# Performance work log

Hardware: AMD Instinct MI355X
Metric: run time of the kernel (lower is better)

## Reference

```python
import jax, jax.numpy as jnp
import numpy as np

C = 256
NH = 8
DH = C // NH
LN_EPS = 1e-5
COS_EPS = 1e-6


def _ln(x, w, b):
    m = x.mean(axis=-1, keepdims=True)
    v = ((x - m) ** 2).mean(axis=-1, keepdims=True)
    return (x - m) / jnp.sqrt(v + LN_EPS) * w + b


def _mha(q_in, kv_in, in_proj_w, in_proj_b, out_proj_w, out_proj_b):
    # q_in, kv_in: [P, S, C]. torch.nn.MultiheadAttention (batch_first).
    P, S, _ = q_in.shape
    q = q_in @ in_proj_w[:C].T + in_proj_b[:C]
    k = kv_in @ in_proj_w[C:2 * C].T + in_proj_b[C:2 * C]
    v = kv_in @ in_proj_w[2 * C:].T + in_proj_b[2 * C:]
    q = q.reshape(P, S, NH, DH)
    k = k.reshape(P, S, NH, DH)
    v = v.reshape(P, S, NH, DH)
    scores = jnp.einsum('pqhd,pkhd->phqk', q, k) / jnp.sqrt(jnp.asarray(DH, q.dtype))
    attn = jax.nn.softmax(scores, axis=-1)
    ctx = jnp.einsum('phqk,pkhd->pqhd', attn, v).reshape(P, S, C)
    return ctx @ out_proj_w.T + out_proj_b


def setup_inputs() -> dict:
    key = jax.random.key(0)
    ks = jax.random.split(key, 8)
    s = 0.02
    return {
        'z_sem': jax.random.normal(ks[0], (16, C, 32, 32), jnp.float32),
        'pair_indices': jnp.arange(16, dtype=jnp.int32).reshape(8, 2),
        'ln_w': jnp.ones((C,), jnp.float32),
        'ln_b': jnp.zeros((C,), jnp.float32),
        'in_proj_w': jax.random.normal(ks[1], (3 * C, C), jnp.float32) * s,
        'in_proj_b': jnp.zeros((3 * C,), jnp.float32),
        'out_proj_w': jax.random.normal(ks[2], (C, C), jnp.float32) * s,
        'out_proj_b': jnp.zeros((C,), jnp.float32),
        'res_scale': jnp.asarray(0.1, jnp.float32),
        'gate_scale': jnp.asarray(2.0, jnp.float32),
        'mlp_ln_w': jnp.ones((C,), jnp.float32),
        'mlp_ln_b': jnp.zeros((C,), jnp.float32),
        'mlp_w1': jax.random.normal(ks[3], (4 * C, C), jnp.float32) * s,
        'mlp_b1': jnp.zeros((4 * C,), jnp.float32),
        'mlp_w2': jax.random.normal(ks[4], (C, 4 * C), jnp.float32) * s,
        'mlp_b2': jnp.zeros((C,), jnp.float32),
    }


def reference(z_sem, pair_indices, ln_w, ln_b, in_proj_w, in_proj_b,
              out_proj_w, out_proj_b, res_scale, gate_scale,
              mlp_ln_w, mlp_ln_b, mlp_w1, mlp_b1, mlp_w2, mlp_b2):
    B, Cc, Hh, Ww = z_sem.shape
    S = Hh * Ww
    tokens = z_sem.reshape(B, Cc, S).transpose(0, 2, 1)  # [B, S, C]

    i_idx = pair_indices[:, 0]
    j_idx = pair_indices[:, 1]
    base_i = tokens[i_idx]  # [P, S, C]
    base_j = tokens[j_idx]

    q_i = _ln(base_i, ln_w, ln_b)
    q_j = _ln(base_j, ln_w, ln_b)

    cross_i = _mha(q_i, q_j, in_proj_w, in_proj_b, out_proj_w, out_proj_b)
    cross_j = _mha(q_j, q_i, in_proj_w, in_proj_b, out_proj_w, out_proj_b)

    # cosine similarity between mean-pooled normed tokens
    mi = q_i.mean(axis=1)  # [P, C]
    mj = q_j.mean(axis=1)
    ni = mi / jnp.maximum(jnp.linalg.norm(mi, axis=-1, keepdims=True), COS_EPS)
    nj = mj / jnp.maximum(jnp.linalg.norm(mj, axis=-1, keepdims=True), COS_EPS)
    sim = (ni * nj).sum(axis=-1)  # [P]
    gate = jax.nn.sigmoid(gate_scale * sim)  # [P]

    g = (res_scale * gate)[:, None, None]
    new_i = base_i + g * cross_i
    new_j = base_j + g * cross_j

    def _mlp(x):
        h = _ln(x, mlp_ln_w, mlp_ln_b)
        h = jax.nn.gelu(h @ mlp_w1.T + mlp_b1, approximate=False)
        return h @ mlp_w2.T + mlp_b2

    new_i = new_i + _mlp(new_i)
    new_j = new_j + _mlp(new_j)

    updated = tokens.at[i_idx].set(new_i).at[j_idx].set(new_j)
    shared = updated.transpose(0, 2, 1).reshape(B, Cc, Hh, Ww)
    return shared, gate, sim
```

## Files before the change

kernel.cpp:

```cpp
#include <hip/hip_runtime.h>
#include <hip/hip_bf16.h>

#define C_ 256
#define S_ 1024
#define NH_ 8
#define DH_ 32
#define NSIDE 16
#define MTOT (NSIDE * S_)

typedef __hip_bfloat16 bf16;
typedef short bf8_t __attribute__((ext_vector_type(8)));
typedef float f4_t __attribute__((ext_vector_type(4)));

#if __has_builtin(__builtin_amdgcn_exp2f)
#define QSCALE 0.25504167f
__device__ __forceinline__ float fastexp(float x) { return __builtin_amdgcn_exp2f(x); }
#else
#define QSCALE 0.17677669529663689f
__device__ __forceinline__ float fastexp(float x) { return __expf(x); }
#endif

__device__ __forceinline__ float b2f(bf16 x) { return __bfloat162float(x); }
__device__ __forceinline__ bf16 f2b(float x) { return __float2bfloat16(x); }
__device__ __forceinline__ unsigned short f2bu(float x) {
    bf16 h = f2b(x);
    return *reinterpret_cast<unsigned short*>(&h);
}
__device__ __forceinline__ unsigned pack_trunc(float a, float b) {
    return __builtin_amdgcn_perm(__float_as_uint(b), __float_as_uint(a), 0x07060302u);
}

__device__ __forceinline__ float block_sum(float v, float* red) {
#pragma unroll
    for (int off = 1; off < 64; off <<= 1) v += __shfl_xor(v, off);
    __syncthreads();
    if ((threadIdx.x & 63) == 0) red[threadIdx.x >> 6] = v;
    __syncthreads();
    return red[0] + red[1] + red[2] + red[3];
}

__device__ __forceinline__ void packone(const float* __restrict__ src, bf16* __restrict__ dst,
                                        int i, int kshift) {
    int n = i >> kshift, k = i & ((1 << kshift) - 1);
    size_t a = ((size_t)((n >> 4) * (1 << (kshift - 5)) + (k >> 5)) << 9) +
               (((k >> 3) & 3) << 7) + ((n & 15) << 3) + (k & 7);
    dst[a] = f2b(src[i]);
}

__global__ void pack4(const float* __restrict__ a, bf16* __restrict__ oa,
                      const float* __restrict__ b, bf16* __restrict__ ob,
                      const float* __restrict__ c, bf16* __restrict__ oc,
                      const float* __restrict__ d, bf16* __restrict__ od) {
    int i = blockIdx.x * blockDim.x + threadIdx.x;
    if (i < 196608) { packone(a, oa, i, 8); return; }
    i -= 196608;
    if (i < 65536) { packone(b, ob, i, 8); return; }
    i -= 65536;
    if (i < 262144) { packone(c, oc, i, 8); return; }
    i -= 262144;
    if (i < 262144) packone(d, od, i, 10);
}

__global__ __launch_bounds__(256) void ln_tokens_g(const float* __restrict__ src,
                                                   const int* __restrict__ pair,
                                                   const float* __restrict__ w,
                                                   const float* __restrict__ b,
                                                   bf16* __restrict__ dst) {
    __shared__ float psum[4][64], psq[4][64], mean_s[64], rstd_s[64];
    __shared__ float wb[512];
    int sb = blockIdx.x, u = blockIdx.y;
    int bi = pair[u];
    int tid = threadIdx.x;
    wb[tid] = w[tid];
    wb[256 + tid] = b[tid];
    int sl = tid & 63, cp = tid >> 6;
    int s = sb * 64 + sl;
    const float* zb = src + (size_t)bi * C_ * S_ + s;
    float sum = 0.f, sq = 0.f;
    for (int c = cp * 64; c < cp * 64 + 64; ++c) {
        float x = zb[(size_t)c * S_];
        sum += x;
        sq += x * x;
    }
    psum[cp][sl] = sum;
    psq[cp][sl] = sq;
    __syncthreads();
    if (tid < 64) {
        float sm = psum[0][tid] + psum[1][tid] + psum[2][tid] + psum[3][tid];
        float q2 = psq[0][tid] + psq[1][tid] + psq[2][tid] + psq[3][tid];
        float mean = sm * (1.0f / C_);
        float var = q2 * (1.0f / C_) - mean * mean;
        mean_s[tid] = mean;
        rstd_s[tid] = rsqrtf(var + 1e-5f);
    }
    __syncthreads();
    float mean = mean_s[sl], rstd = rstd_s[sl];
    int m = u * S_ + s;
    size_t tile8 = (size_t)(m >> 4) * 8;
    for (int c8 = 0; c8 < 64; c8 += 8) {
        int c = cp * 64 + c8;
        bf8_t pk;
#pragma unroll
        for (int j = 0; j < 8; ++j) {
            float x = zb[(size_t)(c + j) * S_];
            float y = (x - mean) * rstd * wb[c + j] + wb[256 + c + j];
            pk[j] = (short)f2bu(y);
        }
        *reinterpret_cast<bf8_t*>(dst + ((tile8 + (c >> 5)) << 9) +
                                  (((c >> 3) & 3) << 7) + ((m & 15) << 3)) = pk;
    }
}

__global__ __launch_bounds__(256) void mean_partial(const bf16* __restrict__ qln,
                                                    float* __restrict__ partial) {
    int u = blockIdx.y, sy = blockIdx.x;
    int c = threadIdx.x;
    float sum = 0.f;
    int s0 = sy * 128;
    int inner = (((c >> 3) & 3) << 7) + (c & 7);
    for (int a = 0; a < 8; ++a) {
        const bf16* p = qln + ((((size_t)u * 64 + (s0 >> 4) + a) * 8 + (c >> 5)) << 9) + inner;
#pragma unroll
        for (int bq = 0; bq < 16; ++bq) sum += b2f(p[bq << 3]);
    }
    partial[(u * 8 + sy) * C_ + c] = sum;
}

__global__ __launch_bounds__(256) void gate_kernel(const float* __restrict__ partial,
                                                   const float* __restrict__ gate_scale,
                                                   float* __restrict__ gatef,
                                                   float* __restrict__ out_gate,
                                                   float* __restrict__ out_sim) {
    __shared__ float red[4];
    int p = blockIdx.x, c = threadIdx.x;
    float mi = 0.f, mj = 0.f;
    for (int sy = 0; sy < 8; ++sy) {
        mi += partial[((2 * p) * 8 + sy) * C_ + c];
        mj += partial[((2 * p + 1) * 8 + sy) * C_ + c];
    }
    mi *= (1.f / S_);
    mj *= (1.f / S_);
    float ii = block_sum(mi * mi, red);
    float jj = block_sum(mj * mj, red);
    float ij = block_sum(mi * mj, red);
    if (c == 0) {
        float ni = fmaxf(sqrtf(ii), 1e-6f);
        float nj = fmaxf(sqrtf(jj), 1e-6f);
        float sim = ij / (ni * nj);
        float gate = 1.f / (1.f + expf(-gate_scale[0] * sim));
        gatef[p] = gate;
        out_gate[p] = gate;
        out_sim[p] = sim;
    }
}

__global__ __launch_bounds__(256) void gemm_qkv(
    const bf16* __restrict__ Apk, const bf16* __restrict__ Wpk, const float* __restrict__ bias,
    bf16* __restrict__ qpk, bf16* __restrict__ kpk, bf16* __restrict__ vpk) {
    int tid = threadIdx.x;
    int wv = tid >> 6, lane = tid & 63;
    int ln15 = lane & 15, quad = lane >> 4;
    int idx = blockIdx.x * 4 + wv;
    int mt = idx / 12, nt = idx % 12;
    int m0 = mt * 64, n0 = nt * 64;

    f4_t acc[4][4];
#pragma unroll
    for (int i = 0; i < 4; ++i)
#pragma unroll
        for (int j = 0; j < 4; ++j) acc[i][j] = (f4_t)(0.0f);

    const bf16* Ab = Apk + ((size_t)mt << 14) + lane * 8;
    const bf16* Wb = Wpk + ((size_t)nt << 14) + lane * 8;

    bf8_t a0[4], w0[4], a1[4], w1[4];
#pragma unroll
    for (int i = 0; i < 4; ++i) {
        a0[i] = *reinterpret_cast<const bf8_t*>(Ab + ((size_t)(i * 8) << 9));
        w0[i] = *reinterpret_cast<const bf8_t*>(Wb + ((size_t)(i * 8) << 9));
    }
    for (int kch = 0; kch < 8; kch += 2) {
#pragma unroll
        for (int i = 0; i < 4; ++i) {
            a1[i] = *reinterpret_cast<const bf8_t*>(Ab + ((size_t)(i * 8 + kch + 1) << 9));
            w1[i] = *reinterpret_cast<const bf8_t*>(Wb + ((size_t)(i * 8 + kch + 1) << 9));
        }
#pragma unroll
        for (int i = 0; i < 4; ++i)
#pragma unroll
            for (int j = 0; j < 4; ++j)
                acc[i][j] = __builtin_amdgcn_mfma_f32_16x16x32_bf16(a0[i], w0[j], acc[i][j], 0, 0, 0);
        if (kch + 2 < 8) {
#pragma unroll
            for (int i = 0; i < 4; ++i) {
                a0[i] = *reinterpret_cast<const bf8_t*>(Ab + ((size_t)(i * 8 + kch + 2) << 9));
                w0[i] = *reinterpret_cast<const bf8_t*>(Wb + ((size_t)(i * 8 + kch + 2) << 9));
            }
        }
#pragma unroll
        for (int i = 0; i < 4; ++i)
#pragma unroll
            for (int j = 0; j < 4; ++j)
                acc[i][j] = __builtin_amdgcn_mfma_f32_16x16x32_bf16(a1[i], w1[j], acc[i][j], 0, 0, 0);
    }

#pragma unroll
    for (int i = 0; i < 4; ++i) {
#pragma unroll
        for (int j = 0; j < 4; ++j) {
            int coln = n0 + j * 16 + ln15;
            float bs = bias[coln];
            int row0 = m0 + i * 16 + quad * 4;
            int u = row0 >> 10, s0v = row0 & 1023;
            if (coln < 256) {
                int h = coln >> 5, d = coln & 31;
                bf16* qp = qpk + (((size_t)u * 8 + h) * 1024 + s0v) * 32 + d;
#pragma unroll
                for (int r = 0; r < 4; ++r)
                    qp[r * 32] = f2b((acc[i][j][r] + bs) * QSCALE);
            } else if (coln < 512) {
                int c = coln - 256, h = c >> 5, d = c & 31;
                bf16* kp = kpk + (((size_t)u * 8 + h) * 1024 + s0v) * 32 + d;
#pragma unroll
                for (int r = 0; r < 4; ++r)
                    kp[r * 32] = f2b(acc[i][j][r] + bs);
            } else {
                int c = coln - 512, h = c >> 5, d = c & 31;
                ushort4 pk;
#pragma unroll
                for (int r = 0; r < 4; ++r)
                    ((unsigned short*)&pk)[r] = f2bu(acc[i][j][r] + bs);
                *reinterpret_cast<ushort4*>(
                    vpk + ((((size_t)u * 8 + h) * 32 + (s0v >> 5)) * 32 + d) * 32 + (s0v & 31)) = pk;
            }
        }
    }
}

__global__ __launch_bounds__(256) void attn_mfma(const bf16* __restrict__ qpk,
                                                 const bf16* __restrict__ kpk,
                                                 const bf16* __restrict__ vpk,
                                                 bf16* __restrict__ ctx) {
    __shared__ __align__(16) short smem[4 * 2304];
    int tid = threadIdx.x;
    int wv = tid >> 6, lane = tid & 63;
    int ln15 = lane & 15, quad = lane >> 4;
    int bid = blockIdx.x;
    int g = bid >> 6, rem = bid & 63;
    int qb = rem >> 3, xcd = rem & 7;
    int uh = g * 8 + xcd;
    int u = uh >> 3, h = uh & 7, up = u ^ 3 ^ 2;
    up = (u ^ 1);
    int q0 = qb * 128 + wv * 32;
    short* PL = smem + wv * 2304;

    const bf16* Qb = qpk + (size_t)uh * 32768;
    const bf16* Kb = kpk + ((size_t)(up * 8 + h)) * 32768;
    const bf16* Vb = vpk + ((size_t)(up * 8 + h)) * 32768;

    bf8_t qf[2];
#pragma unroll
    for (int qt = 0; qt < 2; ++qt)
        qf[qt] = *reinterpret_cast<const bf8_t*>(Qb + (size_t)(q0 + qt * 16 + ln15) * 32 + quad * 8);

    bf8_t ones;
#pragma unroll
    for (int t = 0; t < 8; ++t) ones[t] = (short)0x3F80;

    const bf16* kp = Kb + ln15 * 32 + quad * 8;
    const bf16* vp = Vb + ln15 * 32 + quad * 8;
    short* plw = PL + ln15 * 72 + quad * 4;
    const short* plr = PL + ln15 * 72 + quad * 8;

    f4_t o[2][2];
#pragma unroll
    for (int i = 0; i < 2; ++i)
#pragma unroll
        for (int j = 0; j < 2; ++j) o[i][j] = (f4_t)(0.0f);
    f4_t lacc[2];
    lacc[0] = (f4_t)(0.0f);
    lacc[1] = (f4_t)(0.0f);
    f4_t zf = (f4_t)(0.0f);

    for (int it = 0; it < 16; ++it) {
        int k0 = it * 64;
        bf8_t kf[4], vt[2][2];
#pragma unroll
        for (int t = 0; t < 4; ++t)
            kf[t] = *reinterpret_cast<const bf8_t*>(kp + (size_t)(k0 + t * 16) * 32);
#pragma unroll
        for (int kc = 0; kc < 2; ++kc)
#pragma unroll
            for (int dh = 0; dh < 2; ++dh)
                vt[kc][dh] = *reinterpret_cast<const bf8_t*>(vp + (size_t)(it * 2 + kc) * 1024 + dh * 512);

        f4_t st[4][2];
#pragma unroll
        for (int kh = 0; kh < 4; ++kh)
#pragma unroll
            for (int qt = 0; qt < 2; ++qt)
                st[kh][qt] = __builtin_amdgcn_mfma_f32_16x16x32_bf16(kf[kh], qf[qt], zf, 0, 0, 0);

#pragma unroll
        for (int qt = 0; qt < 2; ++qt) {
#pragma unroll
            for (int kh = 0; kh < 4; ++kh) {
                float e0 = fastexp(st[kh][qt][0]);
                float e1 = fastexp(st[kh][qt][1]);
                float e2 = fastexp(st[kh][qt][2]);
                float e3 = fastexp(st[kh][qt][3]);
                uint2 pk;
                pk.x = pack_trunc(e0, e1);
                pk.y = pack_trunc(e2, e3);
                *reinterpret_cast<uint2*>(plw + qt * 1152 + kh * 16) = pk;
            }
        }
#pragma unroll
        for (int qt = 0; qt < 2; ++qt) {
#pragma unroll
            for (int kc = 0; kc < 2; ++kc) {
                bf8_t pf = *reinterpret_cast<const bf8_t*>(plr + qt * 1152 + kc * 32);
                o[0][qt] = __builtin_amdgcn_mfma_f32_16x16x32_bf16(vt[kc][0], pf, o[0][qt], 0, 0, 0);
                o[1][qt] = __builtin_amdgcn_mfma_f32_16x16x32_bf16(vt[kc][1], pf, o[1][qt], 0, 0, 0);
                lacc[qt] = __builtin_amdgcn_mfma_f32_16x16x32_bf16(ones, pf, lacc[qt], 0, 0, 0);
            }
        }
    }

#pragma unroll
    for (int qt = 0; qt < 2; ++qt) {
        float inv = 1.f / lacc[qt][0];
        size_t base = ((size_t)(u * S_ + q0 + qt * 16 + ln15)) * C_ + h * DH_;
#pragma unroll
        for (int dh = 0; dh < 2; ++dh) {
            ushort4 pk;
            pk.x = f2bu(o[dh][qt][0] * inv);
            pk.y = f2bu(o[dh][qt][1] * inv);
            pk.z = f2bu(o[dh][qt][2] * inv);
            pk.w = f2bu(o[dh][qt][3] * inv);
            *reinterpret_cast<ushort4*>(ctx + base + dh * 16 + quad * 4) = pk;
        }
    }
}

__global__ __launch_bounds__(512) void fused_tail(
    const bf16* __restrict__ ctx, const bf16* __restrict__ wout,
    const float* __restrict__ bout, const float* __restrict__ z,
    const int* __restrict__ pair, const float* __restrict__ gatef,
    const float* __restrict__ res_scale,
    const float* __restrict__ lnw, const float* __restrict__ lnb,
    const bf16* __restrict__ w1b, const float* __restrict__ b1,
    const bf16* __restrict__ w2b, const float* __restrict__ b2,
    float* __restrict__ outp) {
    __shared__ __align__(16) short Xs[32][264];
    __shared__ __align__(16) short CHs[32][264];
    __shared__ float ssum[8][32], ssq[8][32], smean[32], srstd[32];

    int tid = threadIdx.x;
    int wv = tid >> 6, lane = tid & 63;
    int ln15 = lane & 15, quad = lane >> 4;
    int u = blockIdx.x >> 5;
    int s0 = (blockIdx.x & 31) * 32;
    int bi = pair[u];
    float g = res_scale[0] * gatef[u >> 1];
    int c0 = wv * 32;

    {
        int row = tid >> 4, col = (tid & 15) * 16;
        const bf16* src = ctx + ((size_t)(u * S_ + s0 + row)) * 256 + col;
        *reinterpret_cast<bf8_t*>(&CHs[row][col]) = *reinterpret_cast<const bf8_t*>(src);
        *reinterpret_cast<bf8_t*>(&CHs[row][col + 8]) = *reinterpret_cast<const bf8_t*>(src + 8);
    }
    __syncthreads();

    f4_t yacc[2][2];
#pragma unroll
    for (int i = 0; i < 2; ++i)
#pragma unroll
        for (int j = 0; j < 2; ++j) yacc[i][j] = (f4_t)(0.0f);
    {
        const bf16* Wb = wout + (((size_t)(wv * 2) * 8) << 9) + lane * 8;
#pragma unroll
        for (int kch = 0; kch < 8; ++kch) {
            bf8_t wf[2], xf[2];
#pragma unroll
            for (int i = 0; i < 2; ++i)
                wf[i] = *reinterpret_cast<const bf8_t*>(Wb + ((size_t)(i * 8 + kch) << 9));
#pragma unroll
            for (int j = 0; j < 2; ++j)
                xf[j] = *reinterpret_cast<const bf8_t*>(&CHs[j * 16 + ln15][kch * 32 + quad * 8]);
#pragma unroll
            for (int i = 0; i < 2; ++i)
#pragma unroll
                for (int j = 0; j < 2; ++j)
                    yacc[i][j] = __builtin_amdgcn_mfma_f32_16x16x32_bf16(wf[i], xf[j], yacc[i][j], 0, 0, 0);
        }
    }
    float psum[2] = {0.f, 0.f}, psq[2] = {0.f, 0.f};
#pragma unroll
    for (int i = 0; i < 2; ++i) {
#pragma unroll
        for (int r = 0; r < 4; ++r) {
            int c = c0 + i * 16 + quad * 4 + r;
            float bs = bout[c];
            const float* zr = z + ((size_t)bi * C_ + c) * S_ + s0;
#pragma unroll
            for (int j = 0; j < 2; ++j) {
                int sl = j * 16 + ln15;
                float y = zr[sl] + g * (yacc[i][j][r] + bs);
                yacc[i][j][r] = y;
                psum[j] += y;
                psq[j] += y * y;
            }
        }
    }
#pragma unroll
    for (int j = 0; j < 2; ++j) {
        psum[j] += __shfl_xor(psum[j], 16);
        psum[j] += __shfl_xor(psum[j], 32);
        psq[j] += __shfl_xor(psq[j], 16);
        psq[j] += __shfl_xor(psq[j], 32);
    }
    if (quad == 0) {
#pragma unroll
        for (int j = 0; j < 2; ++j) {
            ssum[wv][j * 16 + ln15] = psum[j];
            ssq[wv][j * 16 + ln15] = psq[j];
        }
    }
    __syncthreads();
    if (tid < 32) {
        float sm = 0.f, q2 = 0.f;
#pragma unroll
        for (int w = 0; w < 8; ++w) {
            sm += ssum[w][tid];
            q2 += ssq[w][tid];
        }
        float mean = sm * (1.0f / C_);
        float var = q2 * (1.0f / C_) - mean * mean;
        smean[tid] = mean;
        srstd[tid] = rsqrtf(var + 1e-5f);
    }
    __syncthreads();
#pragma unroll
    for (int j = 0; j < 2; ++j) {
        int sl = j * 16 + ln15;
        float mean = smean[sl], rstd = srstd[sl];
#pragma unroll
        for (int i = 0; i < 2; ++i) {
            ushort4 pk;
#pragma unroll
            for (int r = 0; r < 4; ++r) {
                int c = c0 + i * 16 + quad * 4 + r;
                float xv = (yacc[i][j][r] - mean) * rstd * lnw[c] + lnb[c];
                ((unsigned short*)&pk)[r] = f2bu(xv);
            }
            *reinterpret_cast<ushort4*>(&Xs[sl][c0 + i * 16 + quad * 4]) = pk;
        }
    }
    __syncthreads();

    f4_t acc2[2][2];
#pragma unroll
    for (int i = 0; i < 2; ++i)
#pragma unroll
        for (int j = 0; j < 2; ++j) acc2[i][j] = (f4_t)(0.0f);

    for (int pass = 0; pass < 4; ++pass) {
        f4_t hacc[2][2];
#pragma unroll
        for (int i = 0; i < 2; ++i)
#pragma unroll
            for (int j = 0; j < 2; ++j) hacc[i][j] = (f4_t)(0.0f);
        {
            const bf16* W1p = w1b + (((size_t)(pass * 16 + wv * 2) * 8) << 9) + lane * 8;
#pragma unroll
            for (int kch = 0; kch < 8; ++kch) {
                bf8_t wf[2], xf[2];
#pragma unroll
                for (int i = 0; i < 2; ++i)
                    wf[i] = *reinterpret_cast<const bf8_t*>(W1p + ((size_t)(i * 8 + kch) << 9));
#pragma unroll
                for (int j = 0; j < 2; ++j)
                    xf[j] = *reinterpret_cast<const bf8_t*>(&Xs[j * 16 + ln15][kch * 32 + quad * 8]);
#pragma unroll
                for (int i = 0; i < 2; ++i)
#pragma unroll
                    for (int j = 0; j < 2; ++j)
                        hacc[i][j] = __builtin_amdgcn_mfma_f32_16x16x32_bf16(wf[i], xf[j], hacc[i][j], 0, 0, 0);
            }
        }
#pragma unroll
        for (int j = 0; j < 2; ++j) {
#pragma unroll
            for (int i = 0; i < 2; ++i) {
                ushort4 pk;
#pragma unroll
                for (int r = 0; r < 4; ++r) {
                    int hg = pass * 256 + c0 + i * 16 + quad * 4 + r;
                    float v = hacc[i][j][r] + b1[hg];
                    float ge = 0.5f * v * (1.f + erff(v * 0.70710678118f));
                    ((unsigned short*)&pk)[r] = f2bu(ge);
                }
                *reinterpret_cast<ushort4*>(&CHs[j * 16 + ln15][c0 + i * 16 + quad * 4]) = pk;
            }
        }
        __syncthreads();
        {
            const bf16* W2p = w2b + (((size_t)(wv * 2) * 32 + pass * 8) << 9) + lane * 8;
#pragma unroll
            for (int kch = 0; kch < 8; ++kch) {
                bf8_t wf[2], hf[2];
#pragma unroll
                for (int i = 0; i < 2; ++i)
                    wf[i] = *reinterpret_cast<const bf8_t*>(W2p + ((size_t)(i * 32 + kch) << 9));
#pragma unroll
                for (int j = 0; j < 2; ++j)
                    hf[j] = *reinterpret_cast<const bf8_t*>(&CHs[j * 16 + ln15][kch * 32 + quad * 8]);
#pragma unroll
                for (int i = 0; i < 2; ++i)
#pragma unroll
                    for (int j = 0; j < 2; ++j)
                        acc2[i][j] = __builtin_amdgcn_mfma_f32_16x16x32_bf16(wf[i], hf[j], acc2[i][j], 0, 0, 0);
            }
        }
        __syncthreads();
    }

#pragma unroll
    for (int i = 0; i < 2; ++i) {
#pragma unroll
        for (int r = 0; r < 4; ++r) {
            int c = c0 + i * 16 + quad * 4 + r;
            float bs = b2[c];
            float* orow = outp + ((size_t)bi * C_ + c) * S_ + s0;
#pragma unroll
            for (int j = 0; j < 2; ++j)
                orow[j * 16 + ln15] = yacc[i][j][r] + acc2[i][j][r] + bs;
        }
    }
}

extern "C" void kernel_launch(void* const* d_in, const int* in_sizes, int n_in,
                              void* d_out, int out_size, void* d_ws, size_t ws_size,
                              hipStream_t stream) {
    const float* z = (const float*)d_in[0];
    const int* pair = (const int*)d_in[1];
    const float* ln_w = (const float*)d_in[2];
    const float* ln_b = (const float*)d_in[3];
    const float* in_proj_w = (const float*)d_in[4];
    const float* in_proj_b = (const float*)d_in[5];
    const float* out_proj_w = (const float*)d_in[6];
    const float* out_proj_b = (const float*)d_in[7];
    const float* res_scale = (const float*)d_in[8];
    const float* gate_scale = (const float*)d_in[9];
    const float* mlp_ln_w = (const float*)d_in[10];
    const float* mlp_ln_b = (const float*)d_in[11];
    const float* mlp_w1 = (const float*)d_in[12];
    const float* mlp_b1 = (const float*)d_in[13];
    const float* mlp_w2 = (const float*)d_in[14];
    const float* mlp_b2 = (const float*)d_in[15];
    float* out = (float*)d_out;

    char* ws = (char*)d_ws;
    bf16* qln = (bf16*)(ws);
    bf16* qpk = (bf16*)(ws + 8388608);
    bf16* kpk = (bf16*)(ws + 16777216);
    bf16* vpk = (bf16*)(ws + 25165824);
    bf16* ctx = (bf16*)(ws + 33554432);
    bf16* wqkv = (bf16*)(ws + 41943040);
    bf16* wout = (bf16*)(ws + 41943040 + 393216);
    bf16* w1b = (bf16*)(ws + 41943040 + 524288);
    bf16* w2b = (bf16*)(ws + 41943040 + 1048576);
    float* partial = (float*)(ws + 50331648);
    float* gatef = (float*)(ws + 50462720);

    pack4<<<3072, 256, 0, stream>>>(in_proj_w, wqkv, out_proj_w, wout,
                                    mlp_w1, w1b, mlp_w2, w2b);
    ln_tokens_g<<<dim3(16, 16), 256, 0, stream>>>(z, pair, ln_w, ln_b, qln);
    mean_partial<<<dim3(8, 16), 256, 0, stream>>>(qln, partial);
    gate_kernel<<<8, 256, 0, stream>>>(partial, gate_scale, gatef, out + 4194304, out + 4194312);
    gemm_qkv<<<768, 256, 0, stream>>>(qln, wqkv, in_proj_b, qpk, kpk, vpk);
    attn_mfma<<<1024, 256, 0, stream>>>(qpk, kpk, vpk, ctx);
    fused_tail<<<512, 512, 0, stream>>>(ctx, wout, out_proj_b, z, pair, gatef, res_scale,
                                        mlp_ln_w, mlp_ln_b, w1b, mlp_b1, w2b, mlp_b2, out);
}
```

Baseline: 211.1 us.

## Fuse mean pooling into LN kernel and halve attention query tile per block

The LayerNorm kernel now stages its normalized bf16 tile in shared memory and writes per-block channel sums directly, removing the separate mean_partial kernel launch and its re-read of qln. The gate kernel reduces 16 partials instead of 8. The attention kernel processes 16 queries per wave instead of 32 and launches twice as many blocks. This raises parallelism and lowers register and LDS use, but each K/V tile is now loaded twice as often.

```diff
diff --git a/kernel.cpp b/kernel.cpp
--- a/kernel.cpp
+++ b/kernel.cpp
@@ -65,9 +65,11 @@
                                                    const int* __restrict__ pair,
                                                    const float* __restrict__ w,
                                                    const float* __restrict__ b,
-                                                   bf16* __restrict__ dst) {
+                                                   bf16* __restrict__ dst,
+                                                   float* __restrict__ partial) {
     __shared__ float psum[4][64], psq[4][64], mean_s[64], rstd_s[64];
     __shared__ float wb[512];
+    __shared__ __align__(16) short Ys[64][264];
     int sb = blockIdx.x, u = blockIdx.y;
     int bi = pair[u];
     int tid = threadIdx.x;
@@ -106,24 +108,16 @@
             float y = (x - mean) * rstd * wb[c + j] + wb[256 + c + j];
             pk[j] = (short)f2bu(y);
         }
+        *reinterpret_cast<bf8_t*>(&Ys[sl][c]) = pk;
         *reinterpret_cast<bf8_t*>(dst + ((tile8 + (c >> 5)) << 9) +
                                   (((c >> 3) & 3) << 7) + ((m & 15) << 3)) = pk;
     }
-}
-
-__global__ __launch_bounds__(256) void mean_partial(const bf16* __restrict__ qln,
-                                                    float* __restrict__ partial) {
-    int u = blockIdx.y, sy = blockIdx.x;
-    int c = threadIdx.x;
-    float sum = 0.f;
-    int s0 = sy * 128;
-    int inner = (((c >> 3) & 3) << 7) + (c & 7);
-    for (int a = 0; a < 8; ++a) {
-        const bf16* p = qln + ((((size_t)u * 64 + (s0 >> 4) + a) * 8 + (c >> 5)) << 9) + inner;
-#pragma unroll
-        for (int bq = 0; bq < 16; ++bq) sum += b2f(p[bq << 3]);
-    }
-    partial[(u * 8 + sy) * C_ + c] = sum;
+    __syncthreads();
+    float csum = 0.f;
+#pragma unroll 8
+    for (int t = 0; t < 64; ++t)
+        csum += b2f(*reinterpret_cast<const bf16*>(&Ys[t][tid]));
+    partial[((size_t)u * 16 + sb) * C_ + tid] = csum;
 }
 
 __global__ __launch_bounds__(256) void gate_kernel(const float* __restrict__ partial,
@@ -134,9 +128,9 @@
     __shared__ float red[4];
     int p = blockIdx.x, c = threadIdx.x;
     float mi = 0.f, mj = 0.f;
-    for (int sy = 0; sy < 8; ++sy) {
-        mi += partial[((2 * p) * 8 + sy) * C_ + c];
-        mj += partial[((2 * p + 1) * 8 + sy) * C_ + c];
+    for (int sy = 0; sy < 16; ++sy) {
+        mi += partial[((size_t)(2 * p) * 16 + sy) * C_ + c];
+        mj += partial[((size_t)(2 * p + 1) * 16 + sy) * C_ + c];
     }
     mi *= (1.f / S_);
     mj *= (1.f / S_);
@@ -241,27 +235,23 @@
                                                  const bf16* __restrict__ kpk,
                                                  const bf16* __restrict__ vpk,
                                                  bf16* __restrict__ ctx) {
-    __shared__ __align__(16) short smem[4 * 2304];
+    __shared__ __align__(16) short smem[4 * 1152];
     int tid = threadIdx.x;
     int wv = tid >> 6, lane = tid & 63;
     int ln15 = lane & 15, quad = lane >> 4;
     int bid = blockIdx.x;
-    int g = bid >> 6, rem = bid & 63;
+    int g = bid >> 7, rem = bid & 127;
     int qb = rem >> 3, xcd = rem & 7;
     int uh = g * 8 + xcd;
-    int u = uh >> 3, h = uh & 7, up = u ^ 3 ^ 2;
-    up = (u ^ 1);
-    int q0 = qb * 128 + wv * 32;
-    short* PL = smem + wv * 2304;
+    int u = uh >> 3, h = uh & 7, up = u ^ 1;
+    int q0 = qb * 64 + wv * 16;
+    short* PL = smem + wv * 1152;
 
     const bf16* Qb = qpk + (size_t)uh * 32768;
     const bf16* Kb = kpk + ((size_t)(up * 8 + h)) * 32768;
     const bf16* Vb = vpk + ((size_t)(up * 8 + h)) * 32768;
 
-    bf8_t qf[2];
-#pragma unroll
-    for (int qt = 0; qt < 2; ++qt)
-        qf[qt] = *reinterpret_cast<const bf8_t*>(Qb + (size_t)(q0 + qt * 16 + ln15) * 32 + quad * 8);
+    bf8_t qf = *reinterpret_cast<const bf8_t*>(Qb + (size_t)(q0 + ln15) * 32 + quad * 8);
 
     bf8_t ones;
 #pragma unroll
@@ -272,14 +262,10 @@
     short* plw = PL + ln15 * 72 + quad * 4;
     const short* plr = PL + ln15 * 72 + quad * 8;
 
-    f4_t o[2][2];
-#pragma unroll
-    for (int i = 0; i < 2; ++i)
-#pragma unroll
-        for (int j = 0; j < 2; ++j) o[i][j] = (f4_t)(0.0f);
-    f4_t lacc[2];
-    lacc[0] = (f4_t)(0.0f);
-    lacc[1] = (f4_t)(0.0f);
+    f4_t o[2];
+    o[0] = (f4_t)(0.0f);
+    o[1] = (f4_t)(0.0f);
+    f4_t lacc = (f4_t)(0.0f);
     f4_t zf = (f4_t)(0.0f);
 
     for (int it = 0; it < 16; ++it) {
@@ -294,52 +280,41 @@
             for (int dh = 0; dh < 2; ++dh)
                 vt[kc][dh] = *reinterpret_cast<const bf8_t*>(vp + (size_t)(it * 2 + kc) * 1024 + dh * 512);
 
-        f4_t st[4][2];
+        f4_t st[4];
 #pragma unroll
         for (int kh = 0; kh < 4; ++kh)
-#pragma unroll
-            for (int qt = 0; qt < 2; ++qt)
-                st[kh][qt] = __builtin_amdgcn_mfma_f32_16x16x32_bf16(kf[kh], qf[qt], zf, 0, 0, 0);
-
-#pragma unroll
-        for (int qt = 0; qt < 2; ++qt) {
-#pragma unroll
-            for (int kh = 0; kh < 4; ++kh) {
-                float e0 = fastexp(st[kh][qt][0]);
-                float e1 = fastexp(st[kh][qt][1]);
-                float e2 = fastexp(st[kh][qt][2]);
-                float e3 = fastexp(st[kh][qt][3]);
-                uint2 pk;
-                pk.x = pack_trunc(e0, e1);
-                pk.y = pack_trunc(e2, e3);
-                *reinterpret_cast<uint2*>(plw + qt * 1152 + kh * 16) = pk;
-            }
-        }
-#pragma unroll
-        for (int qt = 0; qt < 2; ++qt) {
-#pragma unroll
-            for (int kc = 0; kc < 2; ++kc) {
-                bf8_t pf = *reinterpret_cast<const bf8_t*>(plr + qt * 1152 + kc * 32);
-                o[0][qt] = __builtin_amdgcn_mfma_f32_16x16x32_bf16(vt[kc][0], pf, o[0][qt], 0, 0, 0);
-                o[1][qt] = __builtin_amdgcn_mfma_f32_16x16x32_bf16(vt[kc][1], pf, o[1][qt], 0, 0, 0);
-                lacc[qt] = __builtin_amdgcn_mfma_f32_16x16x32_bf16(ones, pf, lacc[qt], 0, 0, 0);
-            }
-        }
-    }
-
-#pragma unroll
-    for (int qt = 0; qt < 2; ++qt) {
-        float inv = 1.f / lacc[qt][0];
-        size_t base = ((size_t)(u * S_ + q0 + qt * 16 + ln15)) * C_ + h * DH_;
-#pragma unroll
-        for (int dh = 0; dh < 2; ++dh) {
-            ushort4 pk;
-            pk.x = f2bu(o[dh][qt][0] * inv);
-            pk.y = f2bu(o[dh][qt][1] * inv);
-            pk.z = f2bu(o[dh][qt][2] * inv);
-            pk.w = f2bu(o[dh][qt][3] * inv);
-            *reinterpret_cast<ushort4*>(ctx + base + dh * 16 + quad * 4) = pk;
-        }
+            st[kh] = __builtin_amdgcn_mfma_f32_16x16x32_bf16(kf[kh], qf, zf, 0, 0, 0);
+
+#pragma unroll
+        for (int kh = 0; kh < 4; ++kh) {
+            float e0 = fastexp(st[kh][0]);
+            float e1 = fastexp(st[kh][1]);
+            float e2 = fastexp(st[kh][2]);
+            float e3 = fastexp(st[kh][3]);
+            uint2 pk;
+            pk.x = pack_trunc(e0, e1);
+            pk.y = pack_trunc(e2, e3);
+            *reinterpret_cast<uint2*>(plw + kh * 16) = pk;
+        }
+#pragma unroll
+        for (int kc = 0; kc < 2; ++kc) {
+            bf8_t pf = *reinterpret_cast<const bf8_t*>(plr + kc * 32);
+            o[0] = __builtin_amdgcn_mfma_f32_16x16x32_bf16(vt[kc][0], pf, o[0], 0, 0, 0);
+            o[1] = __builtin_amdgcn_mfma_f32_16x16x32_bf16(vt[kc][1], pf, o[1], 0, 0, 0);
+            lacc = __builtin_amdgcn_mfma_f32_16x16x32_bf16(ones, pf, lacc, 0, 0, 0);
+        }
+    }
+
+    float inv = 1.f / lacc[0];
+    size_t base = ((size_t)(u * S_ + q0 + ln15)) * C_ + h * DH_;
+#pragma unroll
+    for (int dh = 0; dh < 2; ++dh) {
+        ushort4 pk;
+        pk.x = f2bu(o[dh][0] * inv);
+        pk.y = f2bu(o[dh][1] * inv);
+        pk.z = f2bu(o[dh][2] * inv);
+        pk.w = f2bu(o[dh][3] * inv);
+        *reinterpret_cast<ushort4*>(ctx + base + dh * 16 + quad * 4) = pk;
     }
 }
 
@@ -573,15 +548,14 @@
     bf16* w1b = (bf16*)(ws + 41943040 + 524288);
     bf16* w2b = (bf16*)(ws + 41943040 + 1048576);
     float* partial = (float*)(ws + 50331648);
-    float* gatef = (float*)(ws + 50462720);
+    float* gatef = (float*)(ws + 50331648 + 262144);
 
     pack4<<<3072, 256, 0, stream>>>(in_proj_w, wqkv, out_proj_w, wout,
                                     mlp_w1, w1b, mlp_w2, w2b);
-    ln_tokens_g<<<dim3(16, 16), 256, 0, stream>>>(z, pair, ln_w, ln_b, qln);
-    mean_partial<<<dim3(8, 16), 256, 0, stream>>>(qln, partial);
+    ln_tokens_g<<<dim3(16, 16), 256, 0, stream>>>(z, pair, ln_w, ln_b, qln, partial);
     gate_kernel<<<8, 256, 0, stream>>>(partial, gate_scale, gatef, out + 4194304, out + 4194312);
     gemm_qkv<<<768, 256, 0, stream>>>(qln, wqkv, in_proj_b, qpk, kpk, vpk);
-    attn_mfma<<<1024, 256, 0, stream>>>(qpk, kpk, vpk, ctx);
+    attn_mfma<<<2048, 256, 0, stream>>>(qpk, kpk, vpk, ctx);
     fused_tail<<<512, 512, 0, stream>>>(ctx, wout, out_proj_b, z, pair, gatef, res_scale,
                                         mlp_ln_w, mlp_ln_b, w1b, mlp_b1, w2b, mlp_b2, out);
 }
```

Result: slower. 243.3 us (+15.2%).

## Fuse token mean pooling into LN kernel and prefetch K/V in attention

Applied to the files above, without the earlier changes.

The LN kernel now stages its normalized bf16 tile in shared memory and writes per-block column sums, which removes the separate mean_partial launch and its re-read of qln. The gate kernel now reduces 16 partials per side instead of 8, and the gate buffer offset moves to fit the larger partial array. The attention loop double-buffers K and V fragments in registers, so the loads for the next iteration are issued before the current softmax and PV MFMAs run. This adds about 33KB of LDS to the LN kernel and more VGPRs to the attention kernel, which could lower occupancy.

```diff
diff --git a/kernel.cpp b/kernel.cpp
--- a/kernel.cpp
+++ b/kernel.cpp
@@ -65,9 +65,11 @@
                                                    const int* __restrict__ pair,
                                                    const float* __restrict__ w,
                                                    const float* __restrict__ b,
-                                                   bf16* __restrict__ dst) {
+                                                   bf16* __restrict__ dst,
+                                                   float* __restrict__ partial) {
     __shared__ float psum[4][64], psq[4][64], mean_s[64], rstd_s[64];
     __shared__ float wb[512];
+    __shared__ __align__(16) short Ys[64][264];
     int sb = blockIdx.x, u = blockIdx.y;
     int bi = pair[u];
     int tid = threadIdx.x;
@@ -106,24 +108,16 @@
             float y = (x - mean) * rstd * wb[c + j] + wb[256 + c + j];
             pk[j] = (short)f2bu(y);
         }
+        *reinterpret_cast<bf8_t*>(&Ys[sl][c]) = pk;
         *reinterpret_cast<bf8_t*>(dst + ((tile8 + (c >> 5)) << 9) +
                                   (((c >> 3) & 3) << 7) + ((m & 15) << 3)) = pk;
     }
-}
-
-__global__ __launch_bounds__(256) void mean_partial(const bf16* __restrict__ qln,
-                                                    float* __restrict__ partial) {
-    int u = blockIdx.y, sy = blockIdx.x;
-    int c = threadIdx.x;
-    float sum = 0.f;
-    int s0 = sy * 128;
-    int inner = (((c >> 3) & 3) << 7) + (c & 7);
-    for (int a = 0; a < 8; ++a) {
-        const bf16* p = qln + ((((size_t)u * 64 + (s0 >> 4) + a) * 8 + (c >> 5)) << 9) + inner;
-#pragma unroll
-        for (int bq = 0; bq < 16; ++bq) sum += b2f(p[bq << 3]);
-    }
-    partial[(u * 8 + sy) * C_ + c] = sum;
+    __syncthreads();
+    float csum = 0.f;
+#pragma unroll 8
+    for (int t = 0; t < 64; ++t)
+        csum += b2f(*reinterpret_cast<const bf16*>(&Ys[t][tid]));
+    partial[((size_t)u * 16 + sb) * C_ + tid] = csum;
 }
 
 __global__ __launch_bounds__(256) void gate_kernel(const float* __restrict__ partial,
@@ -134,9 +128,9 @@
     __shared__ float red[4];
     int p = blockIdx.x, c = threadIdx.x;
     float mi = 0.f, mj = 0.f;
-    for (int sy = 0; sy < 8; ++sy) {
-        mi += partial[((2 * p) * 8 + sy) * C_ + c];
-        mj += partial[((2 * p + 1) * 8 + sy) * C_ + c];
+    for (int sy = 0; sy < 16; ++sy) {
+        mi += partial[((size_t)(2 * p) * 16 + sy) * C_ + c];
+        mj += partial[((size_t)(2 * p + 1) * 16 + sy) * C_ + c];
     }
     mi *= (1.f / S_);
     mj *= (1.f / S_);
@@ -249,8 +243,7 @@
     int g = bid >> 6, rem = bid & 63;
     int qb = rem >> 3, xcd = rem & 7;
     int uh = g * 8 + xcd;
-    int u = uh >> 3, h = uh & 7, up = u ^ 3 ^ 2;
-    up = (u ^ 1);
+    int u = uh >> 3, h = uh & 7, up = u ^ 1;
     int q0 = qb * 128 + wv * 32;
     short* PL = smem + wv * 2304;
 
@@ -282,24 +275,35 @@
     lacc[1] = (f4_t)(0.0f);
     f4_t zf = (f4_t)(0.0f);
 
+    bf8_t kf[4], vt[2][2], kfn[4], vtn[2][2];
+#pragma unroll
+    for (int t = 0; t < 4; ++t)
+        kf[t] = *reinterpret_cast<const bf8_t*>(kp + (size_t)(t * 16) * 32);
+#pragma unroll
+    for (int kc = 0; kc < 2; ++kc)
+#pragma unroll
+        for (int dh = 0; dh < 2; ++dh)
+            vt[kc][dh] = *reinterpret_cast<const bf8_t*>(vp + (size_t)kc * 1024 + dh * 512);
+
     for (int it = 0; it < 16; ++it) {
-        int k0 = it * 64;
-        bf8_t kf[4], vt[2][2];
-#pragma unroll
-        for (int t = 0; t < 4; ++t)
-            kf[t] = *reinterpret_cast<const bf8_t*>(kp + (size_t)(k0 + t * 16) * 32);
-#pragma unroll
-        for (int kc = 0; kc < 2; ++kc)
-#pragma unroll
-            for (int dh = 0; dh < 2; ++dh)
-                vt[kc][dh] = *reinterpret_cast<const bf8_t*>(vp + (size_t)(it * 2 + kc) * 1024 + dh * 512);
-
         f4_t st[4][2];
 #pragma unroll
         for (int kh = 0; kh < 4; ++kh)
 #pragma unroll
             for (int qt = 0; qt < 2; ++qt)
                 st[kh][qt] = __builtin_amdgcn_mfma_f32_16x16x32_bf16(kf[kh], qf[qt], zf, 0, 0, 0);
+
+        if (it < 15) {
+            int k0n = (it + 1) * 64;
+#pragma unroll
+            for (int t = 0; t < 4; ++t)
+                kfn[t] = *reinterpret_cast<const bf8_t*>(kp + (size_t)(k0n + t * 16) * 32);
+#pragma unroll
+            for (int kc = 0; kc < 2; ++kc)
+#pragma unroll
+                for (int dh = 0; dh < 2; ++dh)
+                    vtn[kc][dh] = *reinterpret_cast<const bf8_t*>(vp + (size_t)((it + 1) * 2 + kc) * 1024 + dh * 512);
+        }
 
 #pragma unroll
         for (int qt = 0; qt < 2; ++qt) {
@@ -325,6 +329,12 @@
                 lacc[qt] = __builtin_amdgcn_mfma_f32_16x16x32_bf16(ones, pf, lacc[qt], 0, 0, 0);
             }
         }
+#pragma unroll
+        for (int t = 0; t < 4; ++t) kf[t] = kfn[t];
+#pragma unroll
+        for (int kc = 0; kc < 2; ++kc)
+#pragma unroll
+            for (int dh = 0; dh < 2; ++dh) vt[kc][dh] = vtn[kc][dh];
     }
 
 #pragma unroll
@@ -573,12 +583,11 @@
     bf16* w1b = (bf16*)(ws + 41943040 + 524288);
     bf16* w2b = (bf16*)(ws + 41943040 + 1048576);
     float* partial = (float*)(ws + 50331648);
-    float* gatef = (float*)(ws + 50462720);
+    float* gatef = (float*)(ws + 50331648 + 262144);
 
     pack4<<<3072, 256, 0, stream>>>(in_proj_w, wqkv, out_proj_w, wout,
                                     mlp_w1, w1b, mlp_w2, w2b);
-    ln_tokens_g<<<dim3(16, 16), 256, 0, stream>>>(z, pair, ln_w, ln_b, qln);
-    mean_partial<<<dim3(8, 16), 256, 0, stream>>>(qln, partial);
+    ln_tokens_g<<<dim3(16, 16), 256, 0, stream>>>(z, pair, ln_w, ln_b, qln, partial);
     gate_kernel<<<8, 256, 0, stream>>>(partial, gate_scale, gatef, out + 4194304, out + 4194312);
     gemm_qkv<<<768, 256, 0, stream>>>(qln, wqkv, in_proj_b, qpk, kpk, vpk);
     attn_mfma<<<1024, 256, 0, stream>>>(qpk, kpk, vpk, ctx);
```

New measurement: 214.3 us. About the same (+1.5%).
